# Performance work log

Measured on AMD Instinct MI355X. Metric: run time of the kernel, lower is better.

Reference implementation:

```python
import jax, jax.numpy as jnp
import numpy as np

D1, D2, HIDDEN, BATCH = 8, 8, 256, 131072
SCALE_LIMIT = 1.0


def _mlp(h, w1, b1, w2, b2, w3, b3):
    # Linear-ReLU-Linear-ReLU-Linear, torch Linear convention: y = h @ W.T + b
    h = jax.nn.relu(h @ w1.T + b1)
    h = jax.nn.relu(h @ w2.T + b2)
    return h @ w3.T + b3


def setup_inputs() -> dict:
    key = jax.random.key(0)
    ks = jax.random.split(key, 25)
    inp = {"x": jax.random.normal(ks[0], (BATCH, D1 + D2), dtype=jnp.float32)}
    i = 1
    for net, d_in, d_out in (("s1", D2, D1), ("t1", D2, D1), ("s2", D1, D2), ("t2", D1, D2)):
        for lname, (o, nin) in (("1", (HIDDEN, d_in)), ("2", (HIDDEN, HIDDEN)), ("3", (d_out, HIDDEN))):
            lim = 1.0 / np.sqrt(nin)  # torch default init range
            inp[f"{net}_w{lname}"] = jax.random.uniform(ks[i], (o, nin), jnp.float32, -lim, lim); i += 1
            inp[f"{net}_b{lname}"] = jnp.zeros((o,), jnp.float32)
    return inp


def reference(x,
              s1_w1, s1_b1, s1_w2, s1_b2, s1_w3, s1_b3,
              t1_w1, t1_b1, t1_w2, t1_b2, t1_w3, t1_b3,
              s2_w1, s2_b1, s2_w2, s2_b2, s2_w3, s2_b3,
              t2_w1, t2_b1, t2_w2, t2_b2, t2_w3, t2_b3):
    x1, x2 = x[:, :D1], x[:, D1:]
    # first half-coupling: transform x1 conditioned on x2
    s2 = jnp.tanh(_mlp(x2, s1_w1, s1_b1, s1_w2, s1_b2, s1_w3, s1_b3)) * SCALE_LIMIT
    t2 = _mlp(x2, t1_w1, t1_b1, t1_w2, t1_b2, t1_w3, t1_b3)
    y1 = x1 * jnp.exp(s2) + t2
    # second half-coupling: transform x2 conditioned on y1
    s1 = jnp.tanh(_mlp(y1, s2_w1, s2_b1, s2_w2, s2_b2, s2_w3, s2_b3)) * SCALE_LIMIT
    t1 = _mlp(y1, t2_w1, t2_b1, t2_w2, t2_b2, t2_w3, t2_b3)
    y2 = x2 * jnp.exp(s1) + t1
    y = jnp.concatenate([y1, y2], axis=1)
    log_det = s2.sum(axis=1) + s1.sum(axis=1)
    return y, log_det
```

## Files before the change

kernel.cpp:

```cpp
#include <hip/hip_runtime.h>

#define BATCHN 131072
#define M_TILE 128
#define NTHREADS 1024
#define HPITCH 264
#define W2P_OFF 4096
#define W3P_OFF 73728
#define NET_STRIDE 77824
#define PACK_TOTAL (4 * NET_STRIDE)

typedef _Float16 hv8 __attribute__((ext_vector_type(8)));
typedef _Float16 hv4 __attribute__((ext_vector_type(4)));
typedef __fp16  fp16x2 __attribute__((ext_vector_type(2)));
typedef float f32x16 __attribute__((ext_vector_type(16)));
typedef float f32x4  __attribute__((ext_vector_type(4)));

struct __align__(16) SMEM {
    _Float16 xin[M_TILE][16];
    _Float16 Ha[M_TILE][HPITCH];
    _Float16 Hb[M_TILE][HPITCH];
    float s_tile[M_TILE][8];
    float t_tile[M_TILE][8];
    float ldet[M_TILE];
};

__global__ __launch_bounds__(256) void pack_weights(
    const float* __restrict__ s1w1, const float* __restrict__ s1b1, const float* __restrict__ s1w2, const float* __restrict__ s1b2, const float* __restrict__ s1w3,
    const float* __restrict__ t1w1, const float* __restrict__ t1b1, const float* __restrict__ t1w2, const float* __restrict__ t1b2, const float* __restrict__ t1w3,
    const float* __restrict__ s2w1, const float* __restrict__ s2b1, const float* __restrict__ s2w2, const float* __restrict__ s2b2, const float* __restrict__ s2w3,
    const float* __restrict__ t2w1, const float* __restrict__ t2b1, const float* __restrict__ t2w2, const float* __restrict__ t2b2, const float* __restrict__ t2w3,
    _Float16* __restrict__ wp)
{
    int tid = blockIdx.x * 256 + threadIdx.x;
    if (tid >= PACK_TOTAL) return;
    int net = tid / NET_STRIDE;
    int rem = tid - net * NET_STRIDE;
    const float* w1 = (net == 0) ? s1w1 : (net == 1) ? t1w1 : (net == 2) ? s2w1 : t2w1;
    const float* b1 = (net == 0) ? s1b1 : (net == 1) ? t1b1 : (net == 2) ? s2b1 : t2b1;
    const float* w2 = (net == 0) ? s1w2 : (net == 1) ? t1w2 : (net == 2) ? s2w2 : t2w2;
    const float* b2 = (net == 0) ? s1b2 : (net == 1) ? t1b2 : (net == 2) ? s2b2 : t2b2;
    const float* w3 = (net == 0) ? s1w3 : (net == 1) ? t1w3 : (net == 2) ? s2w3 : t2w3;
    float val;
    if (rem < W2P_OFF) {
        int nt = rem >> 9;
        int l  = (rem >> 3) & 63, j = rem & 7;
        int n  = nt * 32 + (l & 31);
        int k  = ((l >> 5) << 3) + j;
        val = (k < 8) ? w1[n * 8 + k] : (k == 8 ? b1[n] : 0.0f);
    } else if (rem < W3P_OFF) {
        int r = rem - W2P_OFF;
        int chunk = r >> 9;
        int nt = chunk / 17, ks = chunk - nt * 17;
        int l = (r >> 3) & 63, j = r & 7;
        int n = nt * 32 + (l & 31);
        int kk = ((l >> 5) << 3) + j;
        val = (ks < 16) ? w2[n * 256 + ks * 16 + kk] : (kk == 0 ? b2[n] : 0.0f);
    } else {
        int r = rem - W3P_OFF;
        int ks = r >> 9;
        int l = (r >> 3) & 63, j = r & 7;
        int n = l & 15;
        int k = ks * 32 + ((l >> 4) & 3) * 8 + j;
        val = (n < 8) ? w3[n * 256 + k] : 0.0f;
    }
    wp[tid] = (_Float16)val;
}

#define MFMA32(A,B,C) __builtin_amdgcn_mfma_f32_32x32x16_f16((A),(B),(C),0,0,0)

__device__ __forceinline__ void epi4(_Float16* __restrict__ dst, const f32x16& acc)
{
    #pragma unroll
    for (int q = 0; q < 4; ++q) {
        union { hv4 h4; fp16x2 h2[2]; } u;
        u.h2[0] = __builtin_amdgcn_cvt_pkrtz(fmaxf(acc[4*q+0], 0.f), fmaxf(acc[4*q+1], 0.f));
        u.h2[1] = __builtin_amdgcn_cvt_pkrtz(fmaxf(acc[4*q+2], 0.f), fmaxf(acc[4*q+3], 0.f));
        *(hv4*)(dst + 8 * q) = u.h4;
    }
}

__device__ __forceinline__ void layer1(const _Float16* __restrict__ wp, SMEM& sm,
                                       hv8 xb0, hv8 xb1,
                                       int nt, int mt, int lane, int l31, int hi)
{
    hv8 a = *(const hv8*)(wp + nt * 512 + lane * 8);
    f32x16 z = {};
    f32x16 acc0 = MFMA32(a, xb0, z);
    f32x16 acc1 = MFMA32(a, xb1, z);
    epi4(&sm.Ha[mt * 64 + l31][nt * 32 + 4 * hi], acc0);
    epi4(&sm.Ha[mt * 64 + 32 + l31][nt * 32 + 4 * hi], acc1);
}

__device__ __forceinline__ void layer2(const _Float16* __restrict__ wp, SMEM& sm,
                                       int nt, int mt, int lane, int l31, int hi)
{
    const _Float16* __restrict__ w2 = wp + W2P_OFF + nt * (17 * 512);
    hv8 w[17];
    #pragma unroll
    for (int ks = 0; ks < 17; ++ks) w[ks] = *(const hv8*)(w2 + ks * 512 + lane * 8);
    const _Float16* __restrict__ bb0 = &sm.Ha[mt * 64 + l31][hi * 8];
    const _Float16* __restrict__ bb1 = &sm.Ha[mt * 64 + 32 + l31][hi * 8];
    f32x16 acc0 = {}, acc1 = {};
    #pragma unroll
    for (int ks = 0; ks < 17; ++ks) {
        hv8 b0 = *(const hv8*)(bb0 + ks * 16);
        hv8 b1 = *(const hv8*)(bb1 + ks * 16);
        acc0 = MFMA32(w[ks], b0, acc0);
        acc1 = MFMA32(w[ks], b1, acc1);
    }
    epi4(&sm.Hb[mt * 64 + l31][nt * 32 + 4 * hi], acc0);
    epi4(&sm.Hb[mt * 64 + 32 + l31][nt * 32 + 4 * hi], acc1);
}

template <bool IS_S>
__device__ __forceinline__ void layer3(const _Float16* __restrict__ wp, const float* __restrict__ b3,
                                       SMEM& sm, float (*__restrict__ stile)[8],
                                       int wave, int lane)
{
    if (wave >= 8) return;
    const _Float16* __restrict__ w3 = wp + W3P_OFF;
    const int l15 = lane & 15, q = lane >> 4;
    const int m = wave * 16 + l15;
    hv8 w[8];
    #pragma unroll
    for (int ks = 0; ks < 8; ++ks) w[ks] = *(const hv8*)(w3 + ks * 512 + lane * 8);
    const _Float16* __restrict__ bb = &sm.Hb[m][q * 8];
    f32x4 acc = {};
    #pragma unroll
    for (int ks = 0; ks < 8; ++ks)
        acc = __builtin_amdgcn_mfma_f32_16x16x32_f16(w[ks], *(const hv8*)(bb + ks * 32), acc, 0, 0, 0);
    if (q < 2) {
        float4 bv = *(const float4*)(b3 + q * 4);
        float o0 = acc[0] + bv.x, o1 = acc[1] + bv.y, o2 = acc[2] + bv.z, o3 = acc[3] + bv.w;
        if (IS_S) { o0 = tanhf(o0); o1 = tanhf(o1); o2 = tanhf(o2); o3 = tanhf(o3); }
        *(float4*)&stile[m][q * 4] = make_float4(o0, o1, o2, o3);
    }
}

__device__ __forceinline__ void stage(const _Float16* __restrict__ wpS, const float* __restrict__ b3S,
                                      const _Float16* __restrict__ wpT, const float* __restrict__ b3T,
                                      SMEM& sm,
                                      int wave, int nt, int mt, int lane, int l31, int hi)
{
    hv8 xb0 = *(const hv8*)(&sm.xin[mt * 64 + l31][hi * 8]);
    hv8 xb1 = *(const hv8*)(&sm.xin[mt * 64 + 32 + l31][hi * 8]);

    layer1(wpS, sm, xb0, xb1, nt, mt, lane, l31, hi);
    __syncthreads();
    layer2(wpS, sm, nt, mt, lane, l31, hi);
    __syncthreads();
    layer1(wpT, sm, xb0, xb1, nt, mt, lane, l31, hi);
    layer3<true >(wpS, b3S, sm, sm.s_tile, wave, lane);
    __syncthreads();
    layer2(wpT, sm, nt, mt, lane, l31, hi);
    __syncthreads();
    layer3<false>(wpT, b3T, sm, sm.t_tile, wave, lane);
    __syncthreads();
}

__global__ __launch_bounds__(NTHREADS, 4) void coupling_kernel(
    const float* __restrict__ x, const _Float16* __restrict__ wp,
    const float* __restrict__ s1b3, const float* __restrict__ t1b3,
    const float* __restrict__ s2b3, const float* __restrict__ t2b3,
    float* __restrict__ out)
{
    __shared__ SMEM sm;
    const int tid  = threadIdx.x;
    const int wave = tid >> 6, lane = tid & 63;
    const int l31  = lane & 31, hi = lane >> 5;
    const int mt   = wave & 1, nt = wave >> 1;
    const long row0 = (long)blockIdx.x * M_TILE;

    #pragma unroll
    for (int e = tid; e < M_TILE * 16; e += NTHREADS) {
        int row = e >> 4, c = e & 15;
        float v = (c < 8) ? x[(row0 + row) * 16 + 8 + c] : (c == 8 ? 1.0f : 0.0f);
        sm.xin[row][c] = (_Float16)v;
        sm.Ha[row][256 + c] = (c == 0) ? (_Float16)1.0f : (_Float16)0.0f;
    }
    __syncthreads();

    stage(wp + 0 * NET_STRIDE, s1b3, wp + 1 * NET_STRIDE, t1b3, sm, wave, nt, mt, lane, l31, hi);

    {
        int row = tid >> 3, c = tid & 7;
        float s = sm.s_tile[row][c];
        float t = sm.t_tile[row][c];
        float x1 = x[(row0 + row) * 16 + c];
        float y = x1 * expf(s) + t;
        out[(row0 + row) * 16 + c] = y;
        sm.xin[row][c] = (_Float16)y;
    }
    if (tid < M_TILE) {
        float a = 0.f;
        #pragma unroll
        for (int c = 0; c < 8; ++c) a += sm.s_tile[tid][c];
        sm.ldet[tid] = a;
    }
    __syncthreads();

    stage(wp + 2 * NET_STRIDE, s2b3, wp + 3 * NET_STRIDE, t2b3, sm, wave, nt, mt, lane, l31, hi);

    {
        int row = tid >> 3, c = tid & 7;
        float s = sm.s_tile[row][c];
        float t = sm.t_tile[row][c];
        float x2 = x[(row0 + row) * 16 + 8 + c];
        out[(row0 + row) * 16 + 8 + c] = x2 * expf(s) + t;
    }
    if (tid < M_TILE) {
        float a = sm.ldet[tid];
        #pragma unroll
        for (int c = 0; c < 8; ++c) a += sm.s_tile[tid][c];
        out[(long)BATCHN * 16 + row0 + tid] = a;
    }
}

extern "C" void kernel_launch(void* const* d_in, const int* in_sizes, int n_in,
                              void* d_out, int out_size, void* d_ws, size_t ws_size,
                              hipStream_t stream)
{
    const float* x = (const float*)d_in[0];
    const float* s1w1 = (const float*)d_in[1];  const float* s1b1 = (const float*)d_in[2];
    const float* s1w2 = (const float*)d_in[3];  const float* s1b2 = (const float*)d_in[4];
    const float* s1w3 = (const float*)d_in[5];  const float* s1b3 = (const float*)d_in[6];
    const float* t1w1 = (const float*)d_in[7];  const float* t1b1 = (const float*)d_in[8];
    const float* t1w2 = (const float*)d_in[9];  const float* t1b2 = (const float*)d_in[10];
    const float* t1w3 = (const float*)d_in[11]; const float* t1b3 = (const float*)d_in[12];
    const float* s2w1 = (const float*)d_in[13]; const float* s2b1 = (const float*)d_in[14];
    const float* s2w2 = (const float*)d_in[15]; const float* s2b2 = (const float*)d_in[16];
    const float* s2w3 = (const float*)d_in[17]; const float* s2b3 = (const float*)d_in[18];
    const float* t2w1 = (const float*)d_in[19]; const float* t2b1 = (const float*)d_in[20];
    const float* t2w2 = (const float*)d_in[21]; const float* t2b2 = (const float*)d_in[22];
    const float* t2w3 = (const float*)d_in[23]; const float* t2b3 = (const float*)d_in[24];

    _Float16* wp = (_Float16*)d_ws;

    pack_weights<<<(PACK_TOTAL + 255) / 256, 256, 0, stream>>>(
        s1w1, s1b1, s1w2, s1b2, s1w3,
        t1w1, t1b1, t1w2, t1b2, t1w3,
        s2w1, s2b1, s2w2, s2b2, s2w3,
        t2w1, t2b1, t2w2, t2b2, t2w3, wp);

    coupling_kernel<<<BATCHN / M_TILE, NTHREADS, 0, stream>>>(
        x, wp, s1b3, t1b3, s2b3, t2b3, (float*)d_out);
}
```

Baseline: 197.4 us.

## Remap wave tiling to 32 rows by 64 columns in hidden layers

Result: slower. 215.5 us (+9.2%).

```diff
diff --git a/kernel.cpp b/kernel.cpp
--- a/kernel.cpp
+++ b/kernel.cpp
@@ -50,7 +50,9 @@
     } else if (rem < W3P_OFF) {
         int r = rem - W2P_OFF;
         int chunk = r >> 9;
-        int nt = chunk / 17, ks = chunk - nt * 17;
+        int g = chunk / 34, rr = chunk - g * 34;
+        int ks = rr >> 1, s = rr & 1;
+        int nt = 2 * g + s;
         int l = (r >> 3) & 63, j = r & 7;
         int n = nt * 32 + (l & 31);
         int kk = ((l >> 5) << 3) + j;
@@ -80,36 +82,41 @@
 }
 
 __device__ __forceinline__ void layer1(const _Float16* __restrict__ wp, SMEM& sm,
-                                       hv8 xb0, hv8 xb1,
-                                       int nt, int mt, int lane, int l31, int hi)
-{
-    hv8 a = *(const hv8*)(wp + nt * 512 + lane * 8);
+                                       hv8 xb, int g, int h, int lane, int l31, int hi)
+{
+    hv8 a0 = *(const hv8*)(wp + (2 * g + 0) * 512 + lane * 8);
+    hv8 a1 = *(const hv8*)(wp + (2 * g + 1) * 512 + lane * 8);
     f32x16 z = {};
-    f32x16 acc0 = MFMA32(a, xb0, z);
-    f32x16 acc1 = MFMA32(a, xb1, z);
-    epi4(&sm.Ha[mt * 64 + l31][nt * 32 + 4 * hi], acc0);
-    epi4(&sm.Ha[mt * 64 + 32 + l31][nt * 32 + 4 * hi], acc1);
+    f32x16 acc0 = MFMA32(a0, xb, z);
+    f32x16 acc1 = MFMA32(a1, xb, z);
+    const int m = h * 32 + l31;
+    epi4(&sm.Ha[m][g * 64 +      4 * hi], acc0);
+    epi4(&sm.Ha[m][g * 64 + 32 + 4 * hi], acc1);
 }
 
 __device__ __forceinline__ void layer2(const _Float16* __restrict__ wp, SMEM& sm,
-                                       int nt, int mt, int lane, int l31, int hi)
-{
-    const _Float16* __restrict__ w2 = wp + W2P_OFF + nt * (17 * 512);
-    hv8 w[17];
-    #pragma unroll
-    for (int ks = 0; ks < 17; ++ks) w[ks] = *(const hv8*)(w2 + ks * 512 + lane * 8);
-    const _Float16* __restrict__ bb0 = &sm.Ha[mt * 64 + l31][hi * 8];
-    const _Float16* __restrict__ bb1 = &sm.Ha[mt * 64 + 32 + l31][hi * 8];
+                                       int g, int h, int lane, int l31, int hi)
+{
+    const _Float16* __restrict__ w2 = wp + W2P_OFF + g * (34 * 512);
+    hv8 w[34];
+    #pragma unroll
+    for (int i = 0; i < 34; ++i) w[i] = *(const hv8*)(w2 + i * 512 + lane * 8);
+    const int m = h * 32 + l31;
+    const _Float16* __restrict__ bb = &sm.Ha[m][hi * 8];
     f32x16 acc0 = {}, acc1 = {};
     #pragma unroll
-    for (int ks = 0; ks < 17; ++ks) {
-        hv8 b0 = *(const hv8*)(bb0 + ks * 16);
-        hv8 b1 = *(const hv8*)(bb1 + ks * 16);
-        acc0 = MFMA32(w[ks], b0, acc0);
-        acc1 = MFMA32(w[ks], b1, acc1);
-    }
-    epi4(&sm.Hb[mt * 64 + l31][nt * 32 + 4 * hi], acc0);
-    epi4(&sm.Hb[mt * 64 + 32 + l31][nt * 32 + 4 * hi], acc1);
+    for (int ks = 0; ks < 16; ++ks) {
+        hv8 b = *(const hv8*)(bb + ks * 16);
+        acc0 = MFMA32(w[2*ks+0], b, acc0);
+        acc1 = MFMA32(w[2*ks+1], b, acc1);
+    }
+    {
+        hv8 b = *(const hv8*)(&sm.Ha[m][256 + hi * 8]);
+        acc0 = MFMA32(w[32], b, acc0);
+        acc1 = MFMA32(w[33], b, acc1);
+    }
+    epi4(&sm.Hb[m][g * 64 +      4 * hi], acc0);
+    epi4(&sm.Hb[m][g * 64 + 32 + 4 * hi], acc1);
 }
 
 template <bool IS_S>
@@ -140,19 +147,18 @@
 __device__ __forceinline__ void stage(const _Float16* __restrict__ wpS, const float* __restrict__ b3S,
                                       const _Float16* __restrict__ wpT, const float* __restrict__ b3T,
                                       SMEM& sm,
-                                      int wave, int nt, int mt, int lane, int l31, int hi)
-{
-    hv8 xb0 = *(const hv8*)(&sm.xin[mt * 64 + l31][hi * 8]);
-    hv8 xb1 = *(const hv8*)(&sm.xin[mt * 64 + 32 + l31][hi * 8]);
-
-    layer1(wpS, sm, xb0, xb1, nt, mt, lane, l31, hi);
-    __syncthreads();
-    layer2(wpS, sm, nt, mt, lane, l31, hi);
-    __syncthreads();
-    layer1(wpT, sm, xb0, xb1, nt, mt, lane, l31, hi);
+                                      int wave, int g, int h, int lane, int l31, int hi)
+{
+    hv8 xb = *(const hv8*)(&sm.xin[h * 32 + l31][hi * 8]);
+
+    layer1(wpS, sm, xb, g, h, lane, l31, hi);
+    __syncthreads();
+    layer2(wpS, sm, g, h, lane, l31, hi);
+    __syncthreads();
+    layer1(wpT, sm, xb, g, h, lane, l31, hi);
     layer3<true >(wpS, b3S, sm, sm.s_tile, wave, lane);
     __syncthreads();
-    layer2(wpT, sm, nt, mt, lane, l31, hi);
+    layer2(wpT, sm, g, h, lane, l31, hi);
     __syncthreads();
     layer3<false>(wpT, b3T, sm, sm.t_tile, wave, lane);
     __syncthreads();
@@ -168,7 +174,7 @@
     const int tid  = threadIdx.x;
     const int wave = tid >> 6, lane = tid & 63;
     const int l31  = lane & 31, hi = lane >> 5;
-    const int mt   = wave & 1, nt = wave >> 1;
+    const int g    = wave & 3, h = wave >> 2;
     const long row0 = (long)blockIdx.x * M_TILE;
 
     #pragma unroll
@@ -180,7 +186,7 @@
     }
     __syncthreads();
 
-    stage(wp + 0 * NET_STRIDE, s1b3, wp + 1 * NET_STRIDE, t1b3, sm, wave, nt, mt, lane, l31, hi);
+    stage(wp + 0 * NET_STRIDE, s1b3, wp + 1 * NET_STRIDE, t1b3, sm, wave, g, h, lane, l31, hi);
 
     {
         int row = tid >> 3, c = tid & 7;
@@ -199,7 +205,7 @@
     }
     __syncthreads();
 
-    stage(wp + 2 * NET_STRIDE, s2b3, wp + 3 * NET_STRIDE, t2b3, sm, wave, nt, mt, lane, l31, hi);
+    stage(wp + 2 * NET_STRIDE, s2b3, wp + 3 * NET_STRIDE, t2b3, sm, wave, g, h, lane, l31, hi);
 
     {
         int row = tid >> 3, c = tid & 7;
```
